# Kernel optimization log

Measured on AMD Instinct MI355X. Metric: run time of the kernel, lower is better.

Reference implementation:

```python
import jax, jax.numpy as jnp
import numpy as np

B, L, D, H = 2, 2048, 2048, 16
HD = D // H          # head_dim = 128
LD = HD // 4         # latent_dim = 32


def _linear_params(key, fan_in, fan_out):
    kw, kb = jax.random.split(key)
    bound = 1.0 / np.sqrt(fan_in)
    W = jax.random.uniform(kw, (fan_in, fan_out), jnp.float32, -bound, bound)
    b = jax.random.uniform(kb, (fan_out,), jnp.float32, -bound, bound)
    return W, b


def setup_inputs() -> dict:
    key = jax.random.key(0)
    ks = jax.random.split(key, 12)
    x = jax.random.normal(ks[0], (B, L, D), jnp.float32)
    cos = jax.random.uniform(ks[1], (L, HD // 2), jnp.float32)
    sin = jax.random.uniform(ks[2], (L, HD // 2), jnp.float32)
    Wq, bq = _linear_params(ks[3], D, D)
    Wk, bk = _linear_params(ks[4], D, D)
    Wv, bv = _linear_params(ks[5], D, D)
    Wqc, bqc = _linear_params(ks[6], HD, LD)
    Wkc, bkc = _linear_params(ks[7], HD, LD)
    Wvc, bvc = _linear_params(ks[8], HD, LD)
    Wd, bd = _linear_params(ks[9], LD, HD)
    Wo, bo = _linear_params(ks[10], D, D)
    return dict(x=x, cos=cos, sin=sin, Wq=Wq, bq=bq, Wk=Wk, bk=bk, Wv=Wv, bv=bv,
                Wqc=Wqc, bqc=bqc, Wkc=Wkc, bkc=bkc, Wvc=Wvc, bvc=bvc,
                Wd=Wd, bd=bd, Wo=Wo, bo=bo)


def _apply_rope(q, k, cos, sin):
    # q, k: (B, H, L, HD); cos, sin: (L, HD//2) -> broadcast over B, H
    c = cos[None, None, :, :]
    s = sin[None, None, :, :]
    qe, qo = q[..., ::2], q[..., 1::2]
    ke, ko = k[..., ::2], k[..., 1::2]
    q_rot = jnp.stack([qe * c - qo * s, qe * s + qo * c], axis=-1).reshape(q.shape)
    k_rot = jnp.stack([ke * c - ko * s, ke * s + ko * c], axis=-1).reshape(k.shape)
    return q_rot, k_rot


def reference(x, cos, sin, Wq, bq, Wk, bk, Wv, bv,
              Wqc, bqc, Wkc, bkc, Wvc, bvc, Wd, bd, Wo, bo):
    b, l, d = x.shape
    # projections -> (B, H, L, HD)
    q = (x @ Wq + bq).reshape(b, l, H, HD).transpose(0, 2, 1, 3)
    k = (x @ Wk + bk).reshape(b, l, H, HD).transpose(0, 2, 1, 3)
    v = (x @ Wv + bv).reshape(b, l, H, HD).transpose(0, 2, 1, 3)
    q, k = _apply_rope(q, k, cos, sin)
    # low-rank compression into latent_dim
    qc = jnp.einsum('bhld,de->bhle', q, Wqc) + bqc
    kc = jnp.einsum('bhld,de->bhle', k, Wkc) + bkc
    vc = jnp.einsum('bhld,de->bhle', v, Wvc) + bvc
    scores = jnp.einsum('bhqe,bhke->bhqk', qc, kc) / np.sqrt(LD).astype(np.float32)
    causal = jnp.tril(jnp.ones((l, l), dtype=bool))  # True = keep
    scores = jnp.where(causal[None, None], scores, -jnp.inf)
    probs = jax.nn.softmax(scores, axis=-1)
    attn = jnp.einsum('bhqk,bhke->bhqe', probs, vc)
    attn = jnp.einsum('bhle,ed->bhld', attn, Wd) + bd  # decompress to HD
    attn = attn.transpose(0, 2, 1, 3).reshape(b, l, d)
    return attn @ Wo + bo
```

## Files before the change

kernel.cpp:

```cpp
#include <hip/hip_runtime.h>
#include <hip/hip_bf16.h>


#define Bsz 2
#define Lseq 2048
#define Dmod 2048
#define Hn 16
#define HDim 128
#define LDim 32

typedef __bf16 bf16x8 __attribute__((ext_vector_type(8)));
typedef float f32x4 __attribute__((ext_vector_type(4)));
typedef __hip_bfloat16 bf16;

#define GLDS16(g, l)                                                    \
  __builtin_amdgcn_global_load_lds(                                     \
      (const __attribute__((address_space(1))) unsigned int*)(g),       \
      (__attribute__((address_space(3))) unsigned int*)(l), 16, 0, 0)

#define SM_COS 0
#define SM_SIN 131072
#define SM_WC 262144
#define SM_BC 274432
#define SM_WD 274528
#define SM_BD 278624
#define SM_BO 278752
#define SM_BQKV 280800
#define SM_TOT 286944

__device__ inline void conv8(const void* src, size_t so, bf16* dst, size_t dof, int f32) {
  if (f32) {
    const float* s = (const float*)src + so;
    bf16 tmp[8] __attribute__((aligned(16)));
    for (int j = 0; j < 8; ++j) tmp[j] = __float2bfloat16(s[j]);
    *(uint4*)&dst[dof] = *(uint4*)tmp;
  } else {
    *(uint4*)&dst[dof] = *(const uint4*)((const ushort*)src + so);
  }
}

__device__ inline float cv1(const void* s, size_t i, int f32) {
  return f32 ? ((const float*)s)[i] : __bfloat162float(((const bf16*)s)[i]);
}

#define PB_FBP 0
#define PB_T3 256
#define PB_WV 3328
#define PB_CX 5376
#define PB_SM 9472
#define NB_PREP_ALL 9632

__global__ __launch_bounds__(256) void prep_all(
    const void* xS, const void* cosS, const void* sinS, const void* WqS,
    const void* WkS, const void* WvS, const void* WoS, const void* WqcS,
    const void* WkcS, const void* WvcS, const void* bqcS, const void* bkcS,
    const void* bvcS, const void* WdS, const void* bdS, const void* boS,
    const void* bqS, const void* bkS, const void* bvS,
    bf16* __restrict__ xb, bf16* __restrict__ WvB, bf16* __restrict__ WtQK,
    bf16* __restrict__ WtO, bf16* __restrict__ small, bf16* __restrict__ wctG,
    float* __restrict__ bo_part, int* __restrict__ flagW) {
  __shared__ __align__(16) char shm[16640];
  __shared__ int sflag;
  int blk = blockIdx.x;
  int t = threadIdx.x;

  if (t < 64) {
    int bad = 0;
    for (int k = 0; k < 4; ++k) {
      ushort u = ((const ushort*)xS)[t * 4 + k];
      int ex = (u >> 7) & 0xFF;
      if (ex >= 0xC0) bad = 1;
    }
    unsigned long long bl = __ballot(bad);
    if (t == 0) sflag = (bl != 0ULL) ? 1 : 0;
  }
  __syncthreads();
  int f32 = sflag;
  if (blk == 0 && t == 0) *flagW = f32;

  if (blk < PB_T3) {
    float* red = (float*)shm;
    int nb = blk & 15, kb = blk >> 4;
    int col = nb * 128 + (t & 127);
    int half = t >> 7;
    float s = 0.f;
    int kbase = kb * 128 + half * 64;
    for (int i = 0; i < 64; ++i) {
      int k = kbase + i;
      s += cv1(bdS, k & 127, f32) * cv1(WoS, (size_t)k * 2048 + col, f32);
    }
    red[t] = s;
    __syncthreads();
    if (half == 0) bo_part[kb * 2048 + col] = red[t] + red[t + 128];
  } else if (blk < PB_WV) {
    float (*tile)[65] = (float(*)[65])shm;
    int rem0 = blk - PB_T3;
    int z = rem0 >> 10, rem = rem0 & 1023;
    const void* W = (z == 0) ? WqS : (z == 1) ? WkS : WoS;
    bf16* Wt = (z == 2) ? WtO : (WtQK + (size_t)z * 2048 * 2048);
    int n0 = (rem & 31) * 64, k0 = (rem >> 5) * 64;
    int x = (t & 7) * 8, y = t >> 3;
    for (int p = 0; p < 2; ++p) {
      int r = y + p * 32;
      if (f32) {
        const float* src = (const float*)W + (size_t)(k0 + r) * 2048 + n0 + x;
        float4 a = *(const float4*)src;
        float4 b2 = *(const float4*)(src + 4);
        tile[r][x + 0] = a.x; tile[r][x + 1] = a.y; tile[r][x + 2] = a.z; tile[r][x + 3] = a.w;
        tile[r][x + 4] = b2.x; tile[r][x + 5] = b2.y; tile[r][x + 6] = b2.z; tile[r][x + 7] = b2.w;
      } else {
        const ushort* src = (const ushort*)W + (size_t)(k0 + r) * 2048 + n0 + x;
        uint4 u = *(const uint4*)src;
        bf16* e = (bf16*)&u;
        for (int jj = 0; jj < 8; ++jj) tile[r][x + jj] = __bfloat162float(e[jj]);
      }
    }
    __syncthreads();
    for (int p = 0; p < 2; ++p) {
      int n = y + p * 32;
      bf16 tmp[8] __attribute__((aligned(16)));
      for (int jj = 0; jj < 8; ++jj) tmp[jj] = __float2bfloat16(tile[x + jj][n]);
      *(uint4*)&Wt[(size_t)(n0 + n) * 2048 + k0 + x] = *(uint4*)tmp;
    }
  } else if (blk < PB_CX) {
    size_t e = ((size_t)(blk - PB_WV) * 256 + t) * 8;
    conv8(WvS, e, WvB, e, f32);
  } else if (blk < PB_SM) {
    size_t e = ((size_t)(blk - PB_CX) * 256 + t) * 8;
    conv8(xS, e, xb, e, f32);
  } else {
    int tid = (blk - PB_SM) * 256 + t;
    if (tid < SM_TOT / 8) {
      size_t e = (size_t)tid * 8;
      const void* src;
      size_t so;
      if (e < SM_SIN) { src = cosS; so = e - SM_COS; }
      else if (e < SM_WC) { src = sinS; so = e - SM_SIN; }
      else if (e < SM_BC) { size_t r = e - SM_WC; src = (r < 4096) ? WqcS : (r < 8192) ? WkcS : WvcS; so = r & 4095; }
      else if (e < SM_WD) { size_t r = e - SM_BC; src = (r < 32) ? bqcS : (r < 64) ? bkcS : bvcS; so = r & 31; }
      else if (e < SM_BD) { src = WdS; so = e - SM_WD; }
      else if (e < SM_BO) { src = bdS; so = e - SM_BD; }
      else if (e < SM_BQKV) { src = boS; so = e - SM_BO; }
      else { size_t r = e - SM_BQKV; src = (r < 2048) ? bqS : (r < 4096) ? bkS : bvS; so = r & 2047; }
      conv8(src, so, small, e, f32);
    } else {
      int idx = tid - SM_TOT / 8;
      for (int i = idx; i < 12288; i += 40960 - SM_TOT / 8) {
        int reg = i >> 12, rem2 = i & 4095, n = rem2 >> 7, k = rem2 & 127;
        const void* src = (reg == 0) ? WqcS : (reg == 1) ? WkcS : WvcS;
        wctG[i] = __float2bfloat16(cv1(src, (size_t)k * 32 + n, f32));
      }
    }
  }
}

__global__ __launch_bounds__(256) void fold_all(
    const bf16* __restrict__ WvB, const bf16* __restrict__ wctG,
    const bf16* __restrict__ WtO, const bf16* __restrict__ small,
    const void* boS, const float* __restrict__ bo_part, const void* bvS,
    const void* bvcS, const void* WvcS, bf16* __restrict__ Wvt,
    bf16* __restrict__ Wot, float* __restrict__ boF, float* __restrict__ bvF,
    const int* __restrict__ flagp) {
  int blk = blockIdx.x;
  int t = threadIdx.x, lane = t & 63, w = t >> 6;
  int qd = lane >> 4, ln = lane & 15;
  if (blk < 256) {
    int nb = blk & 15, h = blk >> 4;
    f32x4 acc[2][2] = {};
    for (int kt = 0; kt < 4; ++kt) {
      bf16x8 af[2], bfr[2];
      for (int i = 0; i < 2; ++i)
        af[i] = *(const bf16x8*)&wctG[8192 + (i * 16 + ln) * 128 + kt * 32 + qd * 8];
      for (int j = 0; j < 2; ++j)
        bfr[j] = *(const bf16x8*)&WvB[(size_t)(nb * 128 + w * 32 + j * 16 + ln) * 2048 +
                                      h * 128 + kt * 32 + qd * 8];
      for (int i = 0; i < 2; ++i)
        for (int j = 0; j < 2; ++j)
          acc[i][j] = __builtin_amdgcn_mfma_f32_16x16x32_bf16(af[i], bfr[j], acc[i][j], 0, 0, 0);
    }
    for (int i = 0; i < 2; ++i)
      for (int j = 0; j < 2; ++j)
        for (int r = 0; r < 4; ++r) {
          int e = i * 16 + qd * 4 + r;
          int col = nb * 128 + w * 32 + j * 16 + ln;
          Wvt[(size_t)(h * 32 + e) * 2048 + col] = __float2bfloat16(acc[i][j][r]);
        }
  } else if (blk < 512) {
    int rem = blk - 256;
    int mb = rem & 15, h = rem >> 4;
    f32x4 acc[2][2] = {};
    for (int kt = 0; kt < 4; ++kt) {
      bf16x8 af[2], bfr[2];
      for (int i = 0; i < 2; ++i)
        af[i] = *(const bf16x8*)&WtO[(size_t)(mb * 128 + w * 32 + i * 16 + ln) * 2048 +
                                     h * 128 + kt * 32 + qd * 8];
      for (int j = 0; j < 2; ++j)
        bfr[j] = *(const bf16x8*)&small[SM_WD + (j * 16 + ln) * 128 + kt * 32 + qd * 8];
      for (int i = 0; i < 2; ++i)
        for (int j = 0; j < 2; ++j)
          acc[i][j] = __builtin_amdgcn_mfma_f32_16x16x32_bf16(af[i], bfr[j], acc[i][j], 0, 0, 0);
    }
    for (int i = 0; i < 2; ++i)
      for (int j = 0; j < 2; ++j)
        for (int r = 0; r < 4; ++r) {
          int row = mb * 128 + w * 32 + i * 16 + qd * 4 + r;
          int col = h * 32 + j * 16 + ln;
          Wot[(size_t)row * 512 + col] = __float2bfloat16(acc[i][j][r]);
        }
  } else {
    int f32 = *flagp;
    int tid = (blk - 512) * 256 + t;
    if (tid < 2048) {
      float s = cv1(boS, tid, f32);
      for (int kb = 0; kb < 16; ++kb) s += bo_part[kb * 2048 + tid];
      boF[tid] = s;
    } else if (tid < 2560) {
      int j = tid - 2048, h = j >> 5, e = j & 31;
      float s = cv1(bvcS, e, f32);
      for (int hd = 0; hd < 128; ++hd)
        s += cv1(bvS, h * 128 + hd, f32) * cv1(WvcS, (size_t)hd * 32 + e, f32);
      bvF[j] = s;
    }
  }
}

#define ESTR 136
__global__ __launch_bounds__(256) void gemm_qkv(
    const bf16* __restrict__ A, const bf16* __restrict__ Bt,
    const bf16* __restrict__ Wvt, const bf16* __restrict__ small,
    const bf16* __restrict__ wctG, const float* __restrict__ bvF,
    bf16* __restrict__ qc, bf16* __restrict__ kc, bf16* __restrict__ vcT) {
  __shared__ bf16 sh[128 * ESTR];
  const int K = 2048;
  int id = blockIdx.x;
  int t = threadIdx.x;
  int lane = t & 63, w = t >> 6;
  int qd = lane >> 4, ln = lane & 15;

  if (id < 1024) {
    bf16* lA = sh;
    bf16* lB = sh + 4096;
    int bn = id & 31, bm = id >> 5;
    int reg = bn >> 4, h = bn & 15;
    int wm = (w >> 1) * 64, wn = (w & 1) * 64;

    f32x4 acc[4][4] = {};
    const bf16* Ab = A + (size_t)(bm * 128) * K;
    const bf16* Bb = Bt + (size_t)(bn * 128) * K;

    for (int kt = 0; kt < K; kt += 32) {
      for (int p = 0; p < 2; ++p) {
        int slot = t + p * 256;
        int r = slot >> 2, c = (slot & 3) * 8;
        GLDS16(&Ab[(size_t)r * K + kt + c], &lA[slot * 8]);
        GLDS16(&Bb[(size_t)r * K + kt + c], &lB[slot * 8]);
      }
      __syncthreads();
      bf16x8 af[4], bfr[4];
      for (int i = 0; i < 4; ++i) af[i] = *(bf16x8*)&lA[(wm + i * 16 + ln) * 32 + qd * 8];
      for (int j = 0; j < 4; ++j) bfr[j] = *(bf16x8*)&lB[(wn + j * 16 + ln) * 32 + qd * 8];
      for (int i = 0; i < 4; ++i)
        for (int j = 0; j < 4; ++j)
          acc[i][j] = __builtin_amdgcn_mfma_f32_16x16x32_bf16(af[i], bfr[j], acc[i][j], 0, 0, 0);
      __syncthreads();
    }

    for (int j = 0; j < 4; ++j) {
      int col = wn + j * 16 + ln;
      float bv = __bfloat162float(small[SM_BQKV + bn * 128 + col]);
      for (int i = 0; i < 4; ++i)
        for (int r = 0; r < 4; ++r)
          sh[(wm + i * 16 + qd * 4 + r) * ESTR + col] = __float2bfloat16(acc[i][j][r] + bv);
    }
    __syncthreads();

    int r0 = w * 32;
    int b = bm >> 4;
    int bh = b * Hn + h;
    bf16x8 bfr2[2][4];
    for (int nt = 0; nt < 2; ++nt)
      for (int kt = 0; kt < 4; ++kt)
        bfr2[nt][kt] = *(const bf16x8*)&wctG[reg * 4096 + (nt * 16 + ln) * 128 + kt * 32 + qd * 8];
    float bc[2];
    bc[0] = __bfloat162float(small[SM_BC + reg * 32 + ln]);
    bc[1] = __bfloat162float(small[SM_BC + reg * 32 + 16 + ln]);

    for (int mt = 0; mt < 2; ++mt) {
      int lb = r0 + mt * 16 + ln;
      int lg2 = (bm & 15) * 128 + lb;
      f32x4 c2[2] = {};
      for (int kt = 0; kt < 4; ++kt) {
        uint4 u = *(uint4*)&sh[lb * ESTR + kt * 32 + qd * 8];
        bf16* e8 = (bf16*)&u;
        int pbase = kt * 16 + qd * 4;
        uint2 cu = *(const uint2*)&small[SM_COS + (size_t)lg2 * 64 + pbase];
        uint2 su = *(const uint2*)&small[SM_SIN + (size_t)lg2 * 64 + pbase];
        const bf16* cp = (const bf16*)&cu;
        const bf16* sp = (const bf16*)&su;
        for (int j = 0; j < 4; ++j) {
          float cvv = __bfloat162float(cp[j]);
          float svv = __bfloat162float(sp[j]);
          float ev = __bfloat162float(e8[2 * j]);
          float ov = __bfloat162float(e8[2 * j + 1]);
          e8[2 * j] = __float2bfloat16(ev * cvv - ov * svv);
          e8[2 * j + 1] = __float2bfloat16(ev * svv + ov * cvv);
        }
        bf16x8 a = *(bf16x8*)&u;
        c2[0] = __builtin_amdgcn_mfma_f32_16x16x32_bf16(a, bfr2[0][kt], c2[0], 0, 0, 0);
        c2[1] = __builtin_amdgcn_mfma_f32_16x16x32_bf16(a, bfr2[1][kt], c2[1], 0, 0, 0);
      }
      int lgbase = (bm & 15) * 128 + r0 + mt * 16 + qd * 4;
      bf16* dst = (reg == 0) ? qc : kc;
      for (int nt = 0; nt < 2; ++nt)
        for (int r = 0; r < 4; ++r)
          dst[((size_t)bh * Lseq + lgbase + r) * 32 + nt * 16 + ln] =
              __float2bfloat16(c2[nt][r] + bc[nt]);
    }
  } else {
    bf16* lA = sh;
    bf16* lB = sh + 2048;
    int rem = id - 1024;
    int nb = rem & 7, bm = rem >> 3;
    int wm = (w >> 1) * 32, wn = (w & 1) * 32;

    f32x4 acc[2][2] = {};
    const bf16* Ab = A + (size_t)(bm * 64) * K;
    const bf16* Bb = Wvt + (size_t)(nb * 64) * K;

    int r = t >> 2, c = (t & 3) * 8;
    for (int kt = 0; kt < K; kt += 32) {
      GLDS16(&Ab[(size_t)r * K + kt + c], &lA[t * 8]);
      GLDS16(&Bb[(size_t)r * K + kt + c], &lB[t * 8]);
      __syncthreads();
      bf16x8 af[2], bfr[2];
      for (int i = 0; i < 2; ++i) af[i] = *(bf16x8*)&lA[(wm + i * 16 + ln) * 32 + qd * 8];
      for (int j = 0; j < 2; ++j) bfr[j] = *(bf16x8*)&lB[(wn + j * 16 + ln) * 32 + qd * 8];
      for (int i = 0; i < 2; ++i)
        for (int j = 0; j < 2; ++j)
          acc[i][j] = __builtin_amdgcn_mfma_f32_16x16x32_bf16(af[i], bfr[j], acc[i][j], 0, 0, 0);
      __syncthreads();
    }

    int b = bm >> 5;
    for (int j = 0; j < 2; ++j) {
      int n = nb * 64 + wn + j * 16 + ln;
      float bb = bvF[n];
      for (int i = 0; i < 2; ++i) {
        int lloc = (bm & 31) * 64 + wm + i * 16 + qd * 4;
        bf16 p4[4] __attribute__((aligned(8)));
        for (int rr = 0; rr < 4; ++rr) p4[rr] = __float2bfloat16(acc[i][j][rr] + bb);
        *(uint2*)&vcT[((size_t)(b * 512 + n)) * 2048 + lloc] = *(uint2*)p4;
      }
    }
  }
}

__global__ __launch_bounds__(256) void gemm_bias_out(const bf16* __restrict__ A,
                                                     const bf16* __restrict__ Bt,
                                                     const float* __restrict__ bias,
                                                     void* __restrict__ C,
                                                     int M, int N, int K,
                                                     const int* __restrict__ flagp) {
  __shared__ bf16 lA[128 * 32];
  __shared__ bf16 lB[128 * 32];
  int f32out = *flagp;
  int bm = blockIdx.y, bn = blockIdx.x;
  int t = threadIdx.x;
  int lane = t & 63, w = t >> 6;
  int wm = (w >> 1) * 64, wn = (w & 1) * 64;
  int qd = lane >> 4, ln = lane & 15;

  f32x4 acc[4][4] = {};
  const bf16* Ab = A + (size_t)(bm * 128) * K;
  const bf16* Bb = Bt + (size_t)(bn * 128) * K;

  for (int kt = 0; kt < K; kt += 32) {
    for (int p = 0; p < 2; ++p) {
      int slot = t + p * 256;
      int r = slot >> 2, c = (slot & 3) * 8;
      GLDS16(&Ab[(size_t)r * K + kt + c], &lA[slot * 8]);
      GLDS16(&Bb[(size_t)r * K + kt + c], &lB[slot * 8]);
    }
    __syncthreads();
    bf16x8 af[4], bfr[4];
    for (int i = 0; i < 4; ++i) af[i] = *(bf16x8*)&lA[(wm + i * 16 + ln) * 32 + qd * 8];
    for (int j = 0; j < 4; ++j) bfr[j] = *(bf16x8*)&lB[(wn + j * 16 + ln) * 32 + qd * 8];
    for (int i = 0; i < 4; ++i)
      for (int j = 0; j < 4; ++j)
        acc[i][j] = __builtin_amdgcn_mfma_f32_16x16x32_bf16(af[i], bfr[j], acc[i][j], 0, 0, 0);
    __syncthreads();
  }
  for (int i = 0; i < 4; ++i)
    for (int j = 0; j < 4; ++j) {
      int col = bn * 128 + wn + j * 16 + ln;
      float bv = bias[col];
      for (int r = 0; r < 4; ++r) {
        int row = bm * 128 + wm + i * 16 + qd * 4 + r;
        float v = acc[i][j][r] + bv;
        if (f32out) ((float*)C)[(size_t)row * N + col] = v;
        else ((bf16*)C)[(size_t)row * N + col] = __float2bfloat16(v);
      }
    }
}

__global__ __launch_bounds__(256) void flash32(const bf16* __restrict__ qc,
                                               const bf16* __restrict__ kc,
                                               const bf16* __restrict__ vcT,
                                               bf16* __restrict__ attn) {
  __shared__ bf16 pbuf[4][16 * 72];
  __shared__ float oL[4][16][33];
  __shared__ float mL[4][16];
  __shared__ float lsL[4][16];
  int t = threadIdx.x;
  int lane = t & 63, w = t >> 6;
  int qd = lane >> 4, ln = lane & 15;
  int blk = blockIdx.x;
  int j = blk & 127;
  int bh = blk >> 7, h = bh & 15, b = bh >> 4;
  int q0 = j * 16;

  bf16x8 qf = *(const bf16x8*)&qc[((size_t)bh * Lseq + q0 + ln) * 32 + qd * 8];

  f32x4 o0 = {}, o1 = {};
  float m[4], ls[4];
  for (int r = 0; r < 4; ++r) { m[r] = -1e30f; ls[r] = 0.f; }
  const float scale2 = 0.17677669529663687f * 1.4426950408889634f;

  int n64 = (q0 + 16 + 63) >> 6;
  int nw = (n64 + 3) >> 2;
  int c0 = w * nw;
  int c1 = min(c0 + nw, n64);

  bf16* pb = pbuf[w];
  bf16x8 kf[4];
  if (c0 < c1) {
    int k0 = c0 * 64;
    for (int c = 0; c < 4; ++c)
      kf[c] = *(const bf16x8*)&kc[((size_t)bh * Lseq + k0 + c * 16 + ln) * 32 + qd * 8];
  }
  for (int ci = c0; ci < c1; ++ci) {
    int k0 = ci * 64;
    f32x4 s[4];
    for (int c = 0; c < 4; ++c) {
      f32x4 z = {};
      s[c] = __builtin_amdgcn_mfma_f32_16x16x32_bf16(qf, kf[c], z, 0, 0, 0);
    }
    size_t vbase = ((size_t)bh * 32 + ln) * Lseq + k0 + qd * 8;
    bf16x8 vf00 = *(const bf16x8*)&vcT[vbase];
    bf16x8 vf01 = *(const bf16x8*)&vcT[vbase + 32];
    bf16x8 vf10 = *(const bf16x8*)&vcT[vbase + (size_t)16 * Lseq];
    bf16x8 vf11 = *(const bf16x8*)&vcT[vbase + (size_t)16 * Lseq + 32];
    if (ci + 1 < c1) {
      int k0n = k0 + 64;
      for (int c = 0; c < 4; ++c)
        kf[c] = *(const bf16x8*)&kc[((size_t)bh * Lseq + k0n + c * 16 + ln) * 32 + qd * 8];
    }
    float sv[4][4];
    for (int r = 0; r < 4; ++r) {
      int qrow = q0 + qd * 4 + r;
      for (int c = 0; c < 4; ++c)
        sv[c][r] = (k0 + c * 16 + ln <= qrow) ? s[c][r] * scale2 : -1e30f;
    }
    for (int r = 0; r < 4; ++r) {
      float mx = fmaxf(fmaxf(sv[0][r], sv[1][r]), fmaxf(sv[2][r], sv[3][r]));
      for (int off = 1; off < 16; off <<= 1) mx = fmaxf(mx, __shfl_xor(mx, off, 64));
      if (!__all(mx <= m[r] + 8.f)) {
        float mn = fmaxf(m[r], mx);
        float alpha = exp2f(m[r] - mn);
        m[r] = mn;
        ls[r] *= alpha;
        o0[r] *= alpha;
        o1[r] *= alpha;
      }
      float rs = 0.f;
      for (int c = 0; c < 4; ++c) { sv[c][r] = exp2f(sv[c][r] - m[r]); rs += sv[c][r]; }
      ls[r] += rs;
    }
    for (int r = 0; r < 4; ++r)
      for (int c = 0; c < 4; ++c)
        pb[(qd * 4 + r) * 72 + c * 16 + ln] = __float2bfloat16(sv[c][r]);
    asm volatile("s_waitcnt lgkmcnt(0)" ::: "memory");
    bf16x8 pf0 = *(bf16x8*)&pb[ln * 72 + qd * 8];
    bf16x8 pf1 = *(bf16x8*)&pb[ln * 72 + 32 + qd * 8];
    o0 = __builtin_amdgcn_mfma_f32_16x16x32_bf16(pf0, vf00, o0, 0, 0, 0);
    o0 = __builtin_amdgcn_mfma_f32_16x16x32_bf16(pf1, vf01, o0, 0, 0, 0);
    o1 = __builtin_amdgcn_mfma_f32_16x16x32_bf16(pf0, vf10, o1, 0, 0, 0);
    o1 = __builtin_amdgcn_mfma_f32_16x16x32_bf16(pf1, vf11, o1, 0, 0, 0);
  }

  for (int r = 0; r < 4; ++r)
    for (int off = 1; off < 16; off <<= 1) ls[r] += __shfl_xor(ls[r], off, 64);

  for (int r = 0; r < 4; ++r) {
    int row = qd * 4 + r;
    oL[w][row][ln] = o0[r];
    oL[w][row][16 + ln] = o1[r];
    if (ln == 0) { mL[w][row] = m[r]; lsL[w][row] = ls[r]; }
  }
  __syncthreads();

  for (int idx = t; idx < 512; idx += 256) {
    int row = idx >> 5, col = idx & 31;
    float m0 = mL[0][row], m1 = mL[1][row], m2 = mL[2][row], m3 = mL[3][row];
    float ms = fmaxf(fmaxf(m0, m1), fmaxf(m2, m3));
    float e0 = exp2f(m0 - ms), e1 = exp2f(m1 - ms);
    float e2 = exp2f(m2 - ms), e3 = exp2f(m3 - ms);
    float lsum = lsL[0][row] * e0 + lsL[1][row] * e1 + lsL[2][row] * e2 + lsL[3][row] * e3;
    float val = oL[0][row][col] * e0 + oL[1][row][col] * e1 +
                oL[2][row][col] * e2 + oL[3][row][col] * e3;
    int l = q0 + row;
    attn[((size_t)(b * Lseq + l)) * 512 + h * 32 + col] = __float2bfloat16(val / lsum);
  }
}

extern "C" void kernel_launch(void* const* d_in, const int* in_sizes, int n_in,
                              void* d_out, int out_size, void* d_ws, size_t ws_size,
                              hipStream_t stream) {
  const void* x = d_in[0];
  const void* cosS = d_in[1];
  const void* sinS = d_in[2];
  const void* Wq = d_in[3];
  const void* bq = d_in[4];
  const void* Wk = d_in[5];
  const void* bk = d_in[6];
  const void* Wv = d_in[7];
  const void* bv = d_in[8];
  const void* Wqc = d_in[9];
  const void* bqc = d_in[10];
  const void* Wkc = d_in[11];
  const void* bkc = d_in[12];
  const void* Wvc = d_in[13];
  const void* bvc = d_in[14];
  const void* Wd = d_in[15];
  const void* bd = d_in[16];
  const void* Wo = d_in[17];
  const void* bo = d_in[18];

  char* ws = (char*)d_ws;
  size_t off = 0;
  auto alloc = [&](size_t bytes) {
    char* p = ws + off;
    off += (bytes + 255) & ~(size_t)255;
    return p;
  };
  int* flag = (int*)alloc(256);
  bf16* small = (bf16*)alloc((size_t)SM_TOT * 2);
  bf16* wctG = (bf16*)alloc((size_t)12288 * 2);
  bf16* xb = (bf16*)alloc((size_t)4096 * 2048 * 2);
  bf16* WvB = (bf16*)alloc((size_t)2048 * 2048 * 2);
  bf16* WtQK = (bf16*)alloc((size_t)4096 * 2048 * 2);
  bf16* WtO = (bf16*)alloc((size_t)2048 * 2048 * 2);
  bf16* Wvt = (bf16*)alloc((size_t)512 * 2048 * 2);
  bf16* Wot = (bf16*)alloc((size_t)2048 * 512 * 2);
  float* bo_part = (float*)alloc((size_t)16 * 2048 * 4);
  float* boF = (float*)alloc((size_t)2048 * 4);
  float* bvF = (float*)alloc((size_t)512 * 4);
  bf16* qcW = (bf16*)alloc((size_t)65536 * 32 * 2);
  bf16* kcW = (bf16*)alloc((size_t)65536 * 32 * 2);
  bf16* vcTW = (bf16*)alloc((size_t)65536 * 32 * 2);
  bf16* attnW = (bf16*)alloc((size_t)4096 * 512 * 2);

  dim3 tb(256);
  prep_all<<<NB_PREP_ALL, tb, 0, stream>>>(
      x, cosS, sinS, Wq, Wk, Wv, Wo, Wqc, Wkc, Wvc, bqc, bkc, bvc, Wd, bd, bo,
      bq, bk, bv, xb, WvB, WtQK, WtO, small, wctG, bo_part, flag);
  fold_all<<<522, tb, 0, stream>>>(WvB, wctG, WtO, small, bo, bo_part, bv, bvc,
                                   Wvc, Wvt, Wot, boF, bvF, flag);
  gemm_qkv<<<1536, tb, 0, stream>>>(xb, WtQK, Wvt, small, wctG, bvF, qcW, kcW, vcTW);
  flash32<<<4096, tb, 0, stream>>>(qcW, kcW, vcTW, attnW);
  gemm_bias_out<<<dim3(16, 32), tb, 0, stream>>>(attnW, Wot, boF, d_out, 4096, 2048,
                                                 512, flag);
}
```

Baseline: 381.0 us.

## Enlarge V-projection GEMM tiles and process 128-key chunks in flash attention

The V-compression GEMM branch now uses 128x128 tiles with a 4x4 MFMA accumulator grid, matching the Q/K branch. This cuts its block count from 512 to 128 and the total grid from 1536 to 1152, raising data reuse per block. The flash kernel now handles 128 keys per iteration instead of 64, with larger K/V register fragments and P buffer. That halves the loop trips and online-softmax rescale checks, but raises register pressure and, for short causal rows, gives coarser work splitting across the four waves.

```diff
diff --git a/kernel.cpp b/kernel.cpp
--- a/kernel.cpp
+++ b/kernel.cpp
@@ -236,13 +236,13 @@
   int t = threadIdx.x;
   int lane = t & 63, w = t >> 6;
   int qd = lane >> 4, ln = lane & 15;
+  bf16* lA = sh;
+  bf16* lB = sh + 4096;
+  int wm = (w >> 1) * 64, wn = (w & 1) * 64;
 
   if (id < 1024) {
-    bf16* lA = sh;
-    bf16* lB = sh + 4096;
     int bn = id & 31, bm = id >> 5;
     int reg = bn >> 4, h = bn & 15;
-    int wm = (w >> 1) * 64, wn = (w & 1) * 64;
 
     f32x4 acc[4][4] = {};
     const bf16* Ab = A + (size_t)(bm * 128) * K;
@@ -317,36 +317,36 @@
               __float2bfloat16(c2[nt][r] + bc[nt]);
     }
   } else {
-    bf16* lA = sh;
-    bf16* lB = sh + 2048;
     int rem = id - 1024;
-    int nb = rem & 7, bm = rem >> 3;
-    int wm = (w >> 1) * 32, wn = (w & 1) * 32;
-
-    f32x4 acc[2][2] = {};
-    const bf16* Ab = A + (size_t)(bm * 64) * K;
-    const bf16* Bb = Wvt + (size_t)(nb * 64) * K;
-
-    int r = t >> 2, c = (t & 3) * 8;
+    int nb = rem & 3, bm = rem >> 2;
+
+    f32x4 acc[4][4] = {};
+    const bf16* Ab = A + (size_t)(bm * 128) * K;
+    const bf16* Bb = Wvt + (size_t)(nb * 128) * K;
+
     for (int kt = 0; kt < K; kt += 32) {
-      GLDS16(&Ab[(size_t)r * K + kt + c], &lA[t * 8]);
-      GLDS16(&Bb[(size_t)r * K + kt + c], &lB[t * 8]);
+      for (int p = 0; p < 2; ++p) {
+        int slot = t + p * 256;
+        int r = slot >> 2, c = (slot & 3) * 8;
+        GLDS16(&Ab[(size_t)r * K + kt + c], &lA[slot * 8]);
+        GLDS16(&Bb[(size_t)r * K + kt + c], &lB[slot * 8]);
+      }
       __syncthreads();
-      bf16x8 af[2], bfr[2];
-      for (int i = 0; i < 2; ++i) af[i] = *(bf16x8*)&lA[(wm + i * 16 + ln) * 32 + qd * 8];
-      for (int j = 0; j < 2; ++j) bfr[j] = *(bf16x8*)&lB[(wn + j * 16 + ln) * 32 + qd * 8];
-      for (int i = 0; i < 2; ++i)
-        for (int j = 0; j < 2; ++j)
+      bf16x8 af[4], bfr[4];
+      for (int i = 0; i < 4; ++i) af[i] = *(bf16x8*)&lA[(wm + i * 16 + ln) * 32 + qd * 8];
+      for (int j = 0; j < 4; ++j) bfr[j] = *(bf16x8*)&lB[(wn + j * 16 + ln) * 32 + qd * 8];
+      for (int i = 0; i < 4; ++i)
+        for (int j = 0; j < 4; ++j)
           acc[i][j] = __builtin_amdgcn_mfma_f32_16x16x32_bf16(af[i], bfr[j], acc[i][j], 0, 0, 0);
       __syncthreads();
     }
 
-    int b = bm >> 5;
-    for (int j = 0; j < 2; ++j) {
-      int n = nb * 64 + wn + j * 16 + ln;
+    int b = bm >> 4;
+    for (int j = 0; j < 4; ++j) {
+      int n = nb * 128 + wn + j * 16 + ln;
       float bb = bvF[n];
-      for (int i = 0; i < 2; ++i) {
-        int lloc = (bm & 31) * 64 + wm + i * 16 + qd * 4;
+      for (int i = 0; i < 4; ++i) {
+        int lloc = (bm & 15) * 128 + wm + i * 16 + qd * 4;
         bf16 p4[4] __attribute__((aligned(8)));
         for (int rr = 0; rr < 4; ++rr) p4[rr] = __float2bfloat16(acc[i][j][rr] + bb);
         *(uint2*)&vcT[((size_t)(b * 512 + n)) * 2048 + lloc] = *(uint2*)p4;
@@ -407,7 +407,7 @@
                                                const bf16* __restrict__ kc,
                                                const bf16* __restrict__ vcT,
                                                bf16* __restrict__ attn) {
-  __shared__ bf16 pbuf[4][16 * 72];
+  __shared__ bf16 pbuf[4][16 * 136];
   __shared__ float oL[4][16][33];
   __shared__ float mL[4][16];
   __shared__ float lsL[4][16];
@@ -426,43 +426,45 @@
   for (int r = 0; r < 4; ++r) { m[r] = -1e30f; ls[r] = 0.f; }
   const float scale2 = 0.17677669529663687f * 1.4426950408889634f;
 
-  int n64 = (q0 + 16 + 63) >> 6;
-  int nw = (n64 + 3) >> 2;
+  int n128 = (q0 + 16 + 127) >> 7;
+  int nw = (n128 + 3) >> 2;
   int c0 = w * nw;
-  int c1 = min(c0 + nw, n64);
+  int c1 = min(c0 + nw, n128);
 
   bf16* pb = pbuf[w];
-  bf16x8 kf[4];
+  bf16x8 kf[8];
   if (c0 < c1) {
-    int k0 = c0 * 64;
-    for (int c = 0; c < 4; ++c)
+    int k0 = c0 * 128;
+    for (int c = 0; c < 8; ++c)
       kf[c] = *(const bf16x8*)&kc[((size_t)bh * Lseq + k0 + c * 16 + ln) * 32 + qd * 8];
   }
   for (int ci = c0; ci < c1; ++ci) {
-    int k0 = ci * 64;
-    f32x4 s[4];
-    for (int c = 0; c < 4; ++c) {
+    int k0 = ci * 128;
+    f32x4 s[8];
+    for (int c = 0; c < 8; ++c) {
       f32x4 z = {};
       s[c] = __builtin_amdgcn_mfma_f32_16x16x32_bf16(qf, kf[c], z, 0, 0, 0);
     }
     size_t vbase = ((size_t)bh * 32 + ln) * Lseq + k0 + qd * 8;
-    bf16x8 vf00 = *(const bf16x8*)&vcT[vbase];
-    bf16x8 vf01 = *(const bf16x8*)&vcT[vbase + 32];
-    bf16x8 vf10 = *(const bf16x8*)&vcT[vbase + (size_t)16 * Lseq];
-    bf16x8 vf11 = *(const bf16x8*)&vcT[vbase + (size_t)16 * Lseq + 32];
+    bf16x8 vf0[4], vf1[4];
+    for (int q = 0; q < 4; ++q) {
+      vf0[q] = *(const bf16x8*)&vcT[vbase + q * 32];
+      vf1[q] = *(const bf16x8*)&vcT[vbase + (size_t)16 * Lseq + q * 32];
+    }
     if (ci + 1 < c1) {
-      int k0n = k0 + 64;
-      for (int c = 0; c < 4; ++c)
+      int k0n = k0 + 128;
+      for (int c = 0; c < 8; ++c)
         kf[c] = *(const bf16x8*)&kc[((size_t)bh * Lseq + k0n + c * 16 + ln) * 32 + qd * 8];
     }
-    float sv[4][4];
+    float sv[8][4];
     for (int r = 0; r < 4; ++r) {
       int qrow = q0 + qd * 4 + r;
-      for (int c = 0; c < 4; ++c)
+      for (int c = 0; c < 8; ++c)
         sv[c][r] = (k0 + c * 16 + ln <= qrow) ? s[c][r] * scale2 : -1e30f;
     }
     for (int r = 0; r < 4; ++r) {
-      float mx = fmaxf(fmaxf(sv[0][r], sv[1][r]), fmaxf(sv[2][r], sv[3][r]));
+      float mx = fmaxf(fmaxf(fmaxf(sv[0][r], sv[1][r]), fmaxf(sv[2][r], sv[3][r])),
+                       fmaxf(fmaxf(sv[4][r], sv[5][r]), fmaxf(sv[6][r], sv[7][r])));
       for (int off = 1; off < 16; off <<= 1) mx = fmaxf(mx, __shfl_xor(mx, off, 64));
       if (!__all(mx <= m[r] + 8.f)) {
         float mn = fmaxf(m[r], mx);
@@ -473,19 +475,18 @@
         o1[r] *= alpha;
       }
       float rs = 0.f;
-      for (int c = 0; c < 4; ++c) { sv[c][r] = exp2f(sv[c][r] - m[r]); rs += sv[c][r]; }
+      for (int c = 0; c < 8; ++c) { sv[c][r] = exp2f(sv[c][r] - m[r]); rs += sv[c][r]; }
       ls[r] += rs;
     }
     for (int r = 0; r < 4; ++r)
-      for (int c = 0; c < 4; ++c)
-        pb[(qd * 4 + r) * 72 + c * 16 + ln] = __float2bfloat16(sv[c][r]);
+      for (int c = 0; c < 8; ++c)
+        pb[(qd * 4 + r) * 136 + c * 16 + ln] = __float2bfloat16(sv[c][r]);
     asm volatile("s_waitcnt lgkmcnt(0)" ::: "memory");
-    bf16x8 pf0 = *(bf16x8*)&pb[ln * 72 + qd * 8];
-    bf16x8 pf1 = *(bf16x8*)&pb[ln * 72 + 32 + qd * 8];
-    o0 = __builtin_amdgcn_mfma_f32_16x16x32_bf16(pf0, vf00, o0, 0, 0, 0);
-    o0 = __builtin_amdgcn_mfma_f32_16x16x32_bf16(pf1, vf01, o0, 0, 0, 0);
-    o1 = __builtin_amdgcn_mfma_f32_16x16x32_bf16(pf0, vf10, o1, 0, 0, 0);
-    o1 = __builtin_amdgcn_mfma_f32_16x16x32_bf16(pf1, vf11, o1, 0, 0, 0);
+    for (int q = 0; q < 4; ++q) {
+      bf16x8 pf = *(bf16x8*)&pb[ln * 136 + q * 32 + qd * 8];
+      o0 = __builtin_amdgcn_mfma_f32_16x16x32_bf16(pf, vf0[q], o0, 0, 0, 0);
+      o1 = __builtin_amdgcn_mfma_f32_16x16x32_bf16(pf, vf1[q], o1, 0, 0, 0);
+    }
   }
 
   for (int r = 0; r < 4; ++r)
@@ -566,7 +567,7 @@
       bq, bk, bv, xb, WvB, WtQK, WtO, small, wctG, bo_part, flag);
   fold_all<<<522, tb, 0, stream>>>(WvB, wctG, WtO, small, bo, bo_part, bv, bvc,
                                    Wvc, Wvt, Wot, boF, bvF, flag);
-  gemm_qkv<<<1536, tb, 0, stream>>>(xb, WtQK, Wvt, small, wctG, bvF, qcW, kcW, vcTW);
+  gemm_qkv<<<1152, tb, 0, stream>>>(xb, WtQK, Wvt, small, wctG, bvF, qcW, kcW, vcTW);
   flash32<<<4096, tb, 0, stream>>>(qcW, kcW, vcTW, attnW);
   gemm_bias_out<<<dim3(16, 32), tb, 0, stream>>>(attnW, Wot, boF, d_out, 4096, 2048,
                                                  512, flag);
```

Measured after the change: 386.2 us. Within noise of the previous version (+1.4%).
